# Kernel optimization log

Hardware: AMD Instinct MI355X
Metric: run time of the kernel (lower is better)

The kernel has to match this reference:

```python
import jax, jax.numpy as jnp
import numpy as np

N, E, H, G, L = 50000, 640000, 128, 8, 3

def setup_inputs() -> dict:
    key = jax.random.key(0)
    ks = jax.random.split(key, 10)
    s = 1.0 / np.sqrt(H)
    return {
        "x": jax.random.normal(ks[0], (N, H), jnp.float32),
        "query": jax.random.normal(ks[1], (G, H), jnp.float32),
        "Wl": jax.random.normal(ks[2], (L, H, H), jnp.float32) * s,
        "bl": jax.random.normal(ks[3], (L, H), jnp.float32) * s,
        "Wr": jax.random.normal(ks[4], (L, H, H), jnp.float32) * s,
        "Wlin": jax.random.normal(ks[5], (H, H), jnp.float32) * s,
        "blin": jax.random.normal(ks[6], (H,), jnp.float32) * s,
        "edge_index": jax.random.randint(ks[7], (2, E), 0, N, jnp.int64),
        "batch_vec": jnp.sort(jax.random.randint(ks[8], (N,), 0, G, jnp.int64)),
    }

def reference(x, query, Wl, bl, Wr, Wlin, blin, edge_index, batch_vec):
    src, dst = edge_index[0], edge_index[1]
    n = x.shape[0]
    for i in range(L):
        # SAGEConv(aggr='max'): gather neighbor feats, scatter-max to dst
        m = jax.ops.segment_max(x[src], dst, num_segments=n)  # [N,H]
        m = jnp.where(jnp.isfinite(m), m, 0.0)  # isolated nodes -> 0 (PyG)
        x = jax.nn.relu(m @ Wl[i].T + bl[i] + x @ Wr[i].T)
    x = x @ Wlin.T + blin  # encoder final linear
    # cosine scoring per graph, vectorized via batch_vec
    xn = x / jnp.linalg.norm(x, axis=1, keepdims=True).clip(1e-12)
    qn = query / jnp.linalg.norm(query, axis=1, keepdims=True).clip(1e-12)
    scores = jnp.sum(xn * qn[batch_vec], axis=1)  # [N]
    return scores
```

## Files before the change

### kernel.cpp

```cpp
#include <hip/hip_runtime.h>
#include <math.h>

#define H 128

typedef _Float16 half8 __attribute__((ext_vector_type(8)));
typedef float f32x16 __attribute__((ext_vector_type(16)));
typedef int int4v __attribute__((ext_vector_type(4)));

__device__ __forceinline__ half8 h8max(half8 a, half8 b) {
#if defined(__has_builtin) && __has_builtin(__builtin_elementwise_max)
    return __builtin_elementwise_max(a, b);
#else
    half8 r;
#pragma unroll
    for (int j = 0; j < 8; ++j) r[j] = a[j] > b[j] ? a[j] : b[j];
    return r;
#endif
}

__device__ __forceinline__ half8 h8shfl_xor(half8 v, int mask) {
    int4v iv;
    __builtin_memcpy(&iv, &v, 16);
#pragma unroll
    for (int j = 0; j < 4; ++j) iv[j] = __shfl_xor(iv[j], mask, 64);
    half8 r;
    __builtin_memcpy(&r, &iv, 16);
    return r;
}


__global__ __launch_bounds__(256) void scan_atomic(const int* __restrict__ deg,
                                                   int* __restrict__ offsets,
                                                   int* __restrict__ gcur, int N) {
    __shared__ int buf[256];
    __shared__ int sbase;
    int tid = threadIdx.x;
    int i = blockIdx.x * 256 + tid;
    int v = (i < N) ? deg[i] : 0;
    int incl = v;
    buf[tid] = v;
    __syncthreads();
#pragma unroll
    for (int off = 1; off < 256; off <<= 1) {
        int t = (tid >= off) ? buf[tid - off] : 0;
        __syncthreads();
        incl += t;
        buf[tid] = incl;
        __syncthreads();
    }
    if (tid == 255) sbase = atomicAdd(gcur, incl);
    __syncthreads();
    if (i < N) offsets[i] = sbase + incl - v;
}

__global__ __launch_bounds__(256) void fill_adj(const int* __restrict__ ei, int E,
                                                const int* __restrict__ offsets,
                                                int* __restrict__ cursor,
                                                int* __restrict__ adj) {
    int e = blockIdx.x * 256 + threadIdx.x;
    if (e < E) {
        int s = ei[e];
        int d = ei[E + e];
        int pos = atomicAdd(&cursor[d], 1);
        adj[offsets[d] + pos] = s;
    }
}


__global__ __launch_bounds__(256) void prep_all(
    const int* __restrict__ ei, int E, int* __restrict__ deg,
    const float* __restrict__ x, const float* __restrict__ query,
    const float* __restrict__ Wl, const float* __restrict__ Wr,
    const float* __restrict__ Wlin, _Float16* __restrict__ xh,
    _Float16* __restrict__ wimg, float* __restrict__ qn, int n8, int HB, int SB,
    int WB) {
    int b = blockIdx.x;
    int tid = threadIdx.x;
    if (b < HB) {
        int e = b * 256 + tid;
        if (e < E) atomicAdd(&deg[ei[E + e]], 1);
    } else if (b < HB + SB) {
        int i = (b - HB) * 256 + tid;
        if (i < n8) {
            const float4* x4 = (const float4*)x;
            float4 u = x4[(size_t)i * 2], v = x4[(size_t)i * 2 + 1];
            float f[8] = {u.x, u.y, u.z, u.w, v.x, v.y, v.z, v.w};
            half8 h;
#pragma unroll
            for (int j = 0; j < 8; ++j) h[j] = (_Float16)f[j];
            *(half8*)(xh + (size_t)i * 8) = h;
        }
    } else if (b < HB + SB + WB) {
        int gidx = (b - HB - SB) * 256 + tid;
        if (gidx < 7 * 2048) {
            int mat = gidx / 2048;
            int rem = gidx - mat * 2048;
            int n = rem >> 4;
            int g = rem & 15;
            const float* src = (mat == 6) ? Wlin
                             : ((mat & 1) ? Wr + (mat >> 1) * H * H
                                          : Wl + (mat >> 1) * H * H);
            const float* p = src + n * H + g * 8;
            half8 h, l;
#pragma unroll
            for (int j = 0; j < 8; ++j) {
                float v = p[j];
                _Float16 hh = (_Float16)v;
                h[j] = hh;
                l[j] = (_Float16)(v - (float)hh);
            }
            int kc4 = g >> 2, gpc = g & 3;
            int posB = (gpc + (n & 3) + ((n >> 2) & 3)) & 3;
            size_t base = (size_t)mat * 32768 + (size_t)kc4 * 8192 + n * 32 + posB * 8;
            *(half8*)(wimg + base) = h;
            *(half8*)(wimg + base + 4096) = l;
        }
    } else {
        int g = b - HB - SB - WB;
        __shared__ float part[4];
        float v = (tid < 128) ? query[g * H + tid] : 0.f;
        float ss = v * v;
#pragma unroll
        for (int off = 32; off > 0; off >>= 1) ss += __shfl_xor(ss, off, 64);
        if ((tid & 63) == 0) part[tid >> 6] = ss;
        __syncthreads();
        float tot = part[0] + part[1];
        if (tid < 128) qn[g * H + tid] = v / fmaxf(sqrtf(tot), 1e-12f);
    }
}


__global__ __launch_bounds__(256) void layer_fused3(
    const half8* __restrict__ Xh, const int* __restrict__ deg,
    const int* __restrict__ offsets, const int* __restrict__ adj,
    const _Float16* __restrict__ Bimg, const float* __restrict__ bias,
    _Float16* __restrict__ Yh, int N) {
    __shared__ __align__(16) _Float16 sU[8192];
    __shared__ __align__(16) _Float16 sB[8192];

    int tid = threadIdx.x;
    int w = tid >> 6;
    int lane = tid & 63;
    int l31 = lane & 31;
    int lhi = lane >> 5;
    int ws = w >> 1;
    int wc = w & 1;
    int n0 = blockIdx.x * 64;

    {
        int sub = lane >> 4;
        int lf = lane & 15;
        const _Float16 ni = (_Float16)(-INFINITY);
        const half8 ninf = {ni, ni, ni, ni, ni, ni, ni, ni};
        const half8 hz = {(_Float16)0.f, (_Float16)0.f, (_Float16)0.f, (_Float16)0.f,
                          (_Float16)0.f, (_Float16)0.f, (_Float16)0.f, (_Float16)0.f};
        int nd = n0 + w * 16 + lf;
        int ndc = nd < N ? nd : N - 1;
        int e0v = offsets[ndc];
        int degv = (nd < N) ? deg[ndc] : 0;

        for (int i = 0; i < 16; ++i) {
            int e0 = __shfl(e0v, i, 64);
            int d = __shfl(degv, i, 64);
            int row = w * 16 + i;
            half8 acc = ninf;
            for (int base = 0; base < d; base += 16) {
                half8 v[4];
#pragma unroll
                for (int q = 0; q < 4; ++q) {
                    int j = base + q * 4 + sub;
                    int idx = adj[e0 + (j < d ? j : d - 1)];
                    v[q] = Xh[(size_t)idx * 16 + lf];
                }
                acc = h8max(acc, h8max(h8max(v[0], v[1]), h8max(v[2], v[3])));
            }
            acc = h8max(acc, h8shfl_xor(acc, 16));
            acc = h8max(acc, h8shfl_xor(acc, 32));
            if (d == 0) acc = hz;
            if (sub == 0) *(half8*)&sU[row * 128 + (lf ^ (row & 15)) * 8] = acc;
        }
    }
    __syncthreads();

    f32x16 acc[2];
#pragma unroll
    for (int nt = 0; nt < 2; ++nt) {
        float bv = bias[wc * 64 + nt * 32 + l31];
#pragma unroll
        for (int r = 0; r < 16; ++r) acc[nt][r] = bv;
    }

    int rl = ws * 32 + l31;

    for (int kc4 = 0; kc4 < 4; ++kc4) {
        if (kc4) __syncthreads();
        {
            const half8* bsrc = (const half8*)(Bimg + (size_t)kc4 * 8192);
            half8* bdst = (half8*)sB;
#pragma unroll
            for (int i = 0; i < 4; ++i) bdst[tid + i * 256] = bsrc[tid + i * 256];
        }
        __syncthreads();
#pragma unroll
        for (int ks = 0; ks < 2; ++ks) {
            int g16 = kc4 * 4 + ks * 2 + lhi;
            int posA = g16 ^ (rl & 15);
            half8 ah = *(const half8*)&sU[rl * 128 + posA * 8];
#pragma unroll
            for (int nt = 0; nt < 2; ++nt) {
                int n = wc * 64 + nt * 32 + l31;
                int gpc = ks * 2 + lhi;
                int posB = (gpc + (n & 3) + ((n >> 2) & 3)) & 3;
                half8 bh = *(const half8*)&sB[n * 32 + posB * 8];
                half8 bl = *(const half8*)&sB[4096 + n * 32 + posB * 8];
                acc[nt] = __builtin_amdgcn_mfma_f32_32x32x16_f16(ah, bh, acc[nt], 0, 0, 0);
                acc[nt] = __builtin_amdgcn_mfma_f32_32x32x16_f16(ah, bl, acc[nt], 0, 0, 0);
            }
        }
    }

    for (int kc4 = 0; kc4 < 4; ++kc4) {
        __syncthreads();
        {
            const half8* bsrc = (const half8*)(Bimg + 32768 + (size_t)kc4 * 8192);
            half8* bdst = (half8*)sB;
#pragma unroll
            for (int i = 0; i < 4; ++i) bdst[tid + i * 256] = bsrc[tid + i * 256];
        }
        if ((kc4 & 1) == 0) {
            int kc64 = kc4 >> 1;
#pragma unroll
            for (int i = 0; i < 2; ++i) {
                int idx = tid + i * 256;
                int row = idx >> 3;
                int gp8 = idx & 7;
                int n = n0 + row;
                half8 h = {(_Float16)0.f, (_Float16)0.f, (_Float16)0.f, (_Float16)0.f,
                           (_Float16)0.f, (_Float16)0.f, (_Float16)0.f, (_Float16)0.f};
                if (n < N) h = Xh[(size_t)n * 16 + kc64 * 8 + gp8];
                int pos8 = (gp8 + (row & 7) + ((row >> 3) & 7)) & 7;
                *(half8*)&sU[row * 72 + pos8 * 8] = h;
            }
        }
        __syncthreads();
#pragma unroll
        for (int ks = 0; ks < 2; ++ks) {
            int gp8 = (kc4 & 1) * 4 + ks * 2 + lhi;
            int posA8 = (gp8 + (rl & 7) + ((rl >> 3) & 7)) & 7;
            half8 ah = *(const half8*)&sU[rl * 72 + posA8 * 8];
#pragma unroll
            for (int nt = 0; nt < 2; ++nt) {
                int n = wc * 64 + nt * 32 + l31;
                int gpc = ks * 2 + lhi;
                int posB = (gpc + (n & 3) + ((n >> 2) & 3)) & 3;
                half8 bh = *(const half8*)&sB[n * 32 + posB * 8];
                half8 bl = *(const half8*)&sB[4096 + n * 32 + posB * 8];
                acc[nt] = __builtin_amdgcn_mfma_f32_32x32x16_f16(ah, bh, acc[nt], 0, 0, 0);
                acc[nt] = __builtin_amdgcn_mfma_f32_32x32x16_f16(ah, bl, acc[nt], 0, 0, 0);
            }
        }
    }

#pragma unroll
    for (int r = 0; r < 16; ++r) {
        int row = n0 + ws * 32 + (r & 3) + 8 * (r >> 2) + 4 * lhi;
        if (row < N) {
#pragma unroll
            for (int nt = 0; nt < 2; ++nt) {
                int col = wc * 64 + nt * 32 + l31;
                Yh[(size_t)row * H + col] = (_Float16)fmaxf(acc[nt][r], 0.f);
            }
        }
    }
}


__global__ __launch_bounds__(256) void final_mfma6(
    const half8* __restrict__ Xh, const _Float16* __restrict__ Bimg,
    const float* __restrict__ blin, const float* __restrict__ qn,
    const int* __restrict__ bv, float* __restrict__ out, int N) {
    __shared__ __align__(16) _Float16 sA[9216];
    __shared__ __align__(16) _Float16 sB[8192];

    int tid = threadIdx.x;
    int w = tid >> 6;
    int lane = tid & 63;
    int l31 = lane & 31;
    int lhi = lane >> 5;
    int n0 = blockIdx.x * 128;

    int arow = n0 + w * 32 + l31;
    arow = arow < N ? arow : N - 1;
    int gl = bv[arow];

    f32x16 acc[4];
#pragma unroll
    for (int nt = 0; nt < 4; ++nt) {
        float b = blin[nt * 32 + l31];
#pragma unroll
        for (int r = 0; r < 16; ++r) acc[nt][r] = b;
    }

    int rl = w * 32 + l31;

    for (int kc4 = 0; kc4 < 4; ++kc4) {
        if (kc4) __syncthreads();
        {
            const half8* bsrc = (const half8*)(Bimg + (size_t)kc4 * 8192);
            half8* bdst = (half8*)sB;
#pragma unroll
            for (int i = 0; i < 4; ++i) bdst[tid + i * 256] = bsrc[tid + i * 256];
        }
        if ((kc4 & 1) == 0) {
            int kc64 = kc4 >> 1;
#pragma unroll
            for (int i = 0; i < 4; ++i) {
                int idx = tid + i * 256;
                int row = idx >> 3;
                int gp8 = idx & 7;
                int n = n0 + row;
                half8 h = {(_Float16)0.f, (_Float16)0.f, (_Float16)0.f, (_Float16)0.f,
                           (_Float16)0.f, (_Float16)0.f, (_Float16)0.f, (_Float16)0.f};
                if (n < N) h = Xh[(size_t)n * 16 + kc64 * 8 + gp8];
                int pos8 = (gp8 + (row & 7) + ((row >> 3) & 7)) & 7;
                *(half8*)&sA[row * 72 + pos8 * 8] = h;
            }
        }
        __syncthreads();
#pragma unroll
        for (int ks = 0; ks < 2; ++ks) {
            int gp8 = (kc4 & 1) * 4 + ks * 2 + lhi;
            int posA8 = (gp8 + (rl & 7) + ((rl >> 3) & 7)) & 7;
            half8 ah = *(const half8*)&sA[rl * 72 + posA8 * 8];
#pragma unroll
            for (int nt = 0; nt < 4; ++nt) {
                int n = nt * 32 + l31;
                int gpc = ks * 2 + lhi;
                int posB = (gpc + (n & 3) + ((n >> 2) & 3)) & 3;
                half8 bh = *(const half8*)&sB[n * 32 + posB * 8];
                half8 bl = *(const half8*)&sB[4096 + n * 32 + posB * 8];
                acc[nt] = __builtin_amdgcn_mfma_f32_32x32x16_f16(ah, bh, acc[nt], 0, 0, 0);
                acc[nt] = __builtin_amdgcn_mfma_f32_32x32x16_f16(ah, bl, acc[nt], 0, 0, 0);
            }
        }
    }

#pragma unroll
    for (int r = 0; r < 16; ++r) {
        int rloc = (r & 3) + 8 * (r >> 2) + 4 * lhi;
        int row = n0 + w * 32 + rloc;
        int g = __shfl(gl, rloc, 32);
        float ss = 0.f, sd = 0.f;
#pragma unroll
        for (int nt = 0; nt < 4; ++nt) {
            float y = acc[nt][r];
            float q = qn[(size_t)g * H + nt * 32 + l31];
            ss = fmaf(y, y, ss);
            sd = fmaf(y, q, sd);
        }
#pragma unroll
        for (int off = 1; off <= 16; off <<= 1) {
            ss += __shfl_xor(ss, off, 64);
            sd += __shfl_xor(sd, off, 64);
        }
        if (l31 == 0 && row < N) out[row] = sd / fmaxf(sqrtf(ss), 1e-12f);
    }
}


extern "C" void kernel_launch(void* const* d_in, const int* in_sizes, int n_in,
                              void* d_out, int out_size, void* d_ws, size_t ws_size,
                              hipStream_t stream) {
    const float* x = (const float*)d_in[0];
    const float* query = (const float*)d_in[1];
    const float* Wl = (const float*)d_in[2];
    const float* bl = (const float*)d_in[3];
    const float* Wr = (const float*)d_in[4];
    const float* Wlin = (const float*)d_in[5];
    const float* blin = (const float*)d_in[6];
    const int* ei = (const int*)d_in[7];
    const int* bv = (const int*)d_in[8];
    float* out = (float*)d_out;

    const int N = in_sizes[0] / H;
    const int E = in_sizes[7] / 2;
    const int G = in_sizes[1] / H;

    char* p = (char*)d_ws;
    auto alloc = [&](size_t bytes) {
        char* r = p;
        p += (bytes + 255) & ~(size_t)255;
        return r;
    };
    int* deg = (int*)alloc((size_t)(2 * N + 1) * sizeof(int));
    int* cursor = deg + N;
    int* gcur = deg + 2 * N;
    int* offsets = (int*)alloc((size_t)N * sizeof(int));
    int* adj = (int*)alloc((size_t)E * sizeof(int));
    float* qn = (float*)alloc((size_t)G * H * sizeof(float));
    _Float16* wimg = (_Float16*)alloc((size_t)7 * 32768 * sizeof(_Float16));
    size_t actH = (size_t)N * H * sizeof(_Float16);
    _Float16* xah = (_Float16*)alloc(actH);
    _Float16* xbh = (_Float16*)alloc(actH);

    hipMemsetAsync(deg, 0, (size_t)(2 * N + 1) * sizeof(int), stream);

    const int n8 = N * H / 8;
    const int HB = (E + 255) / 256;
    const int SB = (n8 + 255) / 256;
    const int WB = (7 * 2048 + 255) / 256;
    prep_all<<<HB + SB + WB + G, 256, 0, stream>>>(ei, E, deg, x, query, Wl, Wr,
                                                   Wlin, xah, wimg, qn, n8, HB,
                                                   SB, WB);
    scan_atomic<<<(N + 255) / 256, 256, 0, stream>>>(deg, offsets, gcur, N);
    fill_adj<<<(E + 255) / 256, 256, 0, stream>>>(ei, E, offsets, cursor, adj);

    const int NGm = (N + 63) / 64;
    const int NGf = (N + 127) / 128;

    layer_fused3<<<NGm, 256, 0, stream>>>(
        (const half8*)xah, deg, offsets, adj, wimg + (size_t)0 * 65536,
        bl + 0 * H, xbh, N);
    layer_fused3<<<NGm, 256, 0, stream>>>(
        (const half8*)xbh, deg, offsets, adj, wimg + (size_t)1 * 65536,
        bl + 1 * H, xah, N);
    layer_fused3<<<NGm, 256, 0, stream>>>(
        (const half8*)xah, deg, offsets, adj, wimg + (size_t)2 * 65536,
        bl + 2 * H, xbh, N);
    final_mfma6<<<NGf, 256, 0, stream>>>(
        (const half8*)xbh, wimg + (size_t)6 * 32768, blin, qn, bv, out, N);
}
```

Baseline: 282.7 us.

## Fuse final linear and cosine scoring into last layer; register-cached adjacency gather

The last SAGE layer kernel is templated so that its FINAL variant writes the ReLU output to shared memory and immediately runs the final linear GEMM and cosine scoring. This removes the separate final kernel and the round trip of the activation through global memory. Separately, when all 16 nodes in a wave group have degree at most 32, adjacency indices are loaded once into registers and distributed via shuffles. That path issues a fixed 8 gathers per node, which adds memory-level parallelism at the cost of some redundant clamped loads.

Result: no change. 283.8 us (+0.4%).

```diff
diff --git a/kernel.cpp b/kernel.cpp
--- a/kernel.cpp
+++ b/kernel.cpp
@@ -130,11 +130,14 @@
 }
 
 
-__global__ __launch_bounds__(256) void layer_fused3(
+template <bool FINAL>
+__global__ __launch_bounds__(256) void layer_fused(
     const half8* __restrict__ Xh, const int* __restrict__ deg,
     const int* __restrict__ offsets, const int* __restrict__ adj,
     const _Float16* __restrict__ Bimg, const float* __restrict__ bias,
-    _Float16* __restrict__ Yh, int N) {
+    _Float16* __restrict__ Yh, const _Float16* __restrict__ BimgF,
+    const float* __restrict__ blin, const float* __restrict__ qn,
+    const int* __restrict__ bv, float* __restrict__ out, int N) {
     __shared__ __align__(16) _Float16 sU[8192];
     __shared__ __align__(16) _Float16 sB[8192];
 
@@ -159,25 +162,65 @@
         int e0v = offsets[ndc];
         int degv = (nd < N) ? deg[ndc] : 0;
 
-        for (int i = 0; i < 16; ++i) {
-            int e0 = __shfl(e0v, i, 64);
-            int d = __shfl(degv, i, 64);
-            int row = w * 16 + i;
-            half8 acc = ninf;
-            for (int base = 0; base < d; base += 16) {
-                half8 v[4];
-#pragma unroll
-                for (int q = 0; q < 4; ++q) {
-                    int j = base + q * 4 + sub;
-                    int idx = adj[e0 + (j < d ? j : d - 1)];
+        int dmx = degv;
+#pragma unroll
+        for (int off = 1; off <= 8; off <<= 1) {
+            int t = __shfl_xor(dmx, off, 64);
+            dmx = t > dmx ? t : dmx;
+        }
+
+        if (dmx <= 32) {
+            int adjf[8];
+#pragma unroll
+            for (int rr = 0; rr < 8; ++rr) {
+                int i = 2 * rr + (lane >> 5);
+                int e0 = __shfl(e0v, i, 64);
+                int d = __shfl(degv, i, 64);
+                int s = lane & 31;
+                int p = d > 0 ? e0 + (s < d ? s : d - 1) : 0;
+                adjf[rr] = adj[p];
+            }
+#pragma unroll
+            for (int i = 0; i < 16; ++i) {
+                int d = __shfl(degv, i, 64);
+                int dm1 = d > 0 ? d - 1 : 0;
+                half8 v[8];
+#pragma unroll
+                for (int q = 0; q < 8; ++q) {
+                    int j = q * 4 + sub;
+                    int jc = j < d ? j : dm1;
+                    int idx = __shfl(adjf[i >> 1], ((i & 1) << 5) | jc, 64);
                     v[q] = Xh[(size_t)idx * 16 + lf];
                 }
-                acc = h8max(acc, h8max(h8max(v[0], v[1]), h8max(v[2], v[3])));
-            }
-            acc = h8max(acc, h8shfl_xor(acc, 16));
-            acc = h8max(acc, h8shfl_xor(acc, 32));
-            if (d == 0) acc = hz;
-            if (sub == 0) *(half8*)&sU[row * 128 + (lf ^ (row & 15)) * 8] = acc;
+                half8 acc = h8max(h8max(h8max(v[0], v[1]), h8max(v[2], v[3])),
+                                  h8max(h8max(v[4], v[5]), h8max(v[6], v[7])));
+                acc = h8max(acc, h8shfl_xor(acc, 16));
+                acc = h8max(acc, h8shfl_xor(acc, 32));
+                if (d == 0) acc = hz;
+                int row = w * 16 + i;
+                if (sub == 0) *(half8*)&sU[row * 128 + ((lf ^ (row & 15)) << 3)] = acc;
+            }
+        } else {
+            for (int i = 0; i < 16; ++i) {
+                int e0 = __shfl(e0v, i, 64);
+                int d = __shfl(degv, i, 64);
+                int row = w * 16 + i;
+                half8 acc = ninf;
+                for (int base = 0; base < d; base += 16) {
+                    half8 v[4];
+#pragma unroll
+                    for (int q = 0; q < 4; ++q) {
+                        int j = base + q * 4 + sub;
+                        int idx = adj[e0 + (j < d ? j : d - 1)];
+                        v[q] = Xh[(size_t)idx * 16 + lf];
+                    }
+                    acc = h8max(acc, h8max(h8max(v[0], v[1]), h8max(v[2], v[3])));
+                }
+                acc = h8max(acc, h8shfl_xor(acc, 16));
+                acc = h8max(acc, h8shfl_xor(acc, 32));
+                if (d == 0) acc = hz;
+                if (sub == 0) *(half8*)&sU[row * 128 + ((lf ^ (row & 15)) << 3)] = acc;
+            }
         }
     }
     __syncthreads();
@@ -185,9 +228,9 @@
     f32x16 acc[2];
 #pragma unroll
     for (int nt = 0; nt < 2; ++nt) {
-        float bv = bias[wc * 64 + nt * 32 + l31];
-#pragma unroll
-        for (int r = 0; r < 16; ++r) acc[nt][r] = bv;
+        float bvv = bias[wc * 64 + nt * 32 + l31];
+#pragma unroll
+        for (int r = 0; r < 16; ++r) acc[nt][r] = bvv;
     }
 
     int rl = ws * 32 + l31;
@@ -212,9 +255,9 @@
                 int gpc = ks * 2 + lhi;
                 int posB = (gpc + (n & 3) + ((n >> 2) & 3)) & 3;
                 half8 bh = *(const half8*)&sB[n * 32 + posB * 8];
-                half8 bl = *(const half8*)&sB[4096 + n * 32 + posB * 8];
+                half8 bl2 = *(const half8*)&sB[4096 + n * 32 + posB * 8];
                 acc[nt] = __builtin_amdgcn_mfma_f32_32x32x16_f16(ah, bh, acc[nt], 0, 0, 0);
-                acc[nt] = __builtin_amdgcn_mfma_f32_32x32x16_f16(ah, bl, acc[nt], 0, 0, 0);
+                acc[nt] = __builtin_amdgcn_mfma_f32_32x32x16_f16(ah, bl2, acc[nt], 0, 0, 0);
             }
         }
     }
@@ -254,116 +297,110 @@
                 int gpc = ks * 2 + lhi;
                 int posB = (gpc + (n & 3) + ((n >> 2) & 3)) & 3;
                 half8 bh = *(const half8*)&sB[n * 32 + posB * 8];
-                half8 bl = *(const half8*)&sB[4096 + n * 32 + posB * 8];
+                half8 bl2 = *(const half8*)&sB[4096 + n * 32 + posB * 8];
                 acc[nt] = __builtin_amdgcn_mfma_f32_32x32x16_f16(ah, bh, acc[nt], 0, 0, 0);
-                acc[nt] = __builtin_amdgcn_mfma_f32_32x32x16_f16(ah, bl, acc[nt], 0, 0, 0);
-            }
-        }
-    }
-
-#pragma unroll
-    for (int r = 0; r < 16; ++r) {
-        int row = n0 + ws * 32 + (r & 3) + 8 * (r >> 2) + 4 * lhi;
-        if (row < N) {
+                acc[nt] = __builtin_amdgcn_mfma_f32_32x32x16_f16(ah, bl2, acc[nt], 0, 0, 0);
+            }
+        }
+    }
+
+    if constexpr (!FINAL) {
+#pragma unroll
+        for (int r = 0; r < 16; ++r) {
+            int row = n0 + ws * 32 + (r & 3) + 8 * (r >> 2) + 4 * lhi;
+            if (row < N) {
+#pragma unroll
+                for (int nt = 0; nt < 2; ++nt) {
+                    int col = wc * 64 + nt * 32 + l31;
+                    Yh[(size_t)row * H + col] = (_Float16)fmaxf(acc[nt][r], 0.f);
+                }
+            }
+        }
+    } else {
+        __syncthreads();
+#pragma unroll
+        for (int r = 0; r < 16; ++r) {
+            int rloc = ws * 32 + (r & 3) + 8 * (r >> 2) + 4 * lhi;
 #pragma unroll
             for (int nt = 0; nt < 2; ++nt) {
-                int col = wc * 64 + nt * 32 + l31;
-                Yh[(size_t)row * H + col] = (_Float16)fmaxf(acc[nt][r], 0.f);
-            }
-        }
-    }
-}
-
-
-__global__ __launch_bounds__(256) void final_mfma6(
-    const half8* __restrict__ Xh, const _Float16* __restrict__ Bimg,
-    const float* __restrict__ blin, const float* __restrict__ qn,
-    const int* __restrict__ bv, float* __restrict__ out, int N) {
-    __shared__ __align__(16) _Float16 sA[9216];
-    __shared__ __align__(16) _Float16 sB[8192];
-
-    int tid = threadIdx.x;
-    int w = tid >> 6;
-    int lane = tid & 63;
-    int l31 = lane & 31;
-    int lhi = lane >> 5;
-    int n0 = blockIdx.x * 128;
-
-    int arow = n0 + w * 32 + l31;
-    arow = arow < N ? arow : N - 1;
-    int gl = bv[arow];
-
-    f32x16 acc[4];
-#pragma unroll
-    for (int nt = 0; nt < 4; ++nt) {
-        float b = blin[nt * 32 + l31];
-#pragma unroll
-        for (int r = 0; r < 16; ++r) acc[nt][r] = b;
-    }
-
-    int rl = w * 32 + l31;
-
-    for (int kc4 = 0; kc4 < 4; ++kc4) {
-        if (kc4) __syncthreads();
-        {
-            const half8* bsrc = (const half8*)(Bimg + (size_t)kc4 * 8192);
-            half8* bdst = (half8*)sB;
-#pragma unroll
-            for (int i = 0; i < 4; ++i) bdst[tid + i * 256] = bsrc[tid + i * 256];
-        }
-        if ((kc4 & 1) == 0) {
-            int kc64 = kc4 >> 1;
-#pragma unroll
-            for (int i = 0; i < 4; ++i) {
-                int idx = tid + i * 256;
-                int row = idx >> 3;
-                int gp8 = idx & 7;
-                int n = n0 + row;
-                half8 h = {(_Float16)0.f, (_Float16)0.f, (_Float16)0.f, (_Float16)0.f,
-                           (_Float16)0.f, (_Float16)0.f, (_Float16)0.f, (_Float16)0.f};
-                if (n < N) h = Xh[(size_t)n * 16 + kc64 * 8 + gp8];
-                int pos8 = (gp8 + (row & 7) + ((row >> 3) & 7)) & 7;
-                *(half8*)&sA[row * 72 + pos8 * 8] = h;
-            }
-        }
-        __syncthreads();
-#pragma unroll
-        for (int ks = 0; ks < 2; ++ks) {
-            int gp8 = (kc4 & 1) * 4 + ks * 2 + lhi;
-            int posA8 = (gp8 + (rl & 7) + ((rl >> 3) & 7)) & 7;
-            half8 ah = *(const half8*)&sA[rl * 72 + posA8 * 8];
-#pragma unroll
-            for (int nt = 0; nt < 4; ++nt) {
-                int n = nt * 32 + l31;
-                int gpc = ks * 2 + lhi;
-                int posB = (gpc + (n & 3) + ((n >> 2) & 3)) & 3;
-                half8 bh = *(const half8*)&sB[n * 32 + posB * 8];
-                half8 bl = *(const half8*)&sB[4096 + n * 32 + posB * 8];
-                acc[nt] = __builtin_amdgcn_mfma_f32_32x32x16_f16(ah, bh, acc[nt], 0, 0, 0);
-                acc[nt] = __builtin_amdgcn_mfma_f32_32x32x16_f16(ah, bl, acc[nt], 0, 0, 0);
-            }
-        }
-    }
-
-#pragma unroll
-    for (int r = 0; r < 16; ++r) {
-        int rloc = (r & 3) + 8 * (r >> 2) + 4 * lhi;
-        int row = n0 + w * 32 + rloc;
-        int g = __shfl(gl, rloc, 32);
-        float ss = 0.f, sd = 0.f;
-#pragma unroll
-        for (int nt = 0; nt < 4; ++nt) {
-            float y = acc[nt][r];
-            float q = qn[(size_t)g * H + nt * 32 + l31];
-            ss = fmaf(y, y, ss);
-            sd = fmaf(y, q, sd);
-        }
-#pragma unroll
-        for (int off = 1; off <= 16; off <<= 1) {
-            ss += __shfl_xor(ss, off, 64);
-            sd += __shfl_xor(sd, off, 64);
-        }
-        if (l31 == 0 && row < N) out[row] = sd / fmaxf(sqrtf(ss), 1e-12f);
+                int c = wc * 64 + nt * 32 + l31;
+                sU[rloc * 128 + (((c >> 3) ^ (rloc & 15)) << 3) + (c & 7)] =
+                    (_Float16)fmaxf(acc[nt][r], 0.f);
+            }
+        }
+
+        f32x16 acc2[2];
+#pragma unroll
+        for (int nt = 0; nt < 2; ++nt) {
+            float b = blin[wc * 64 + nt * 32 + l31];
+#pragma unroll
+            for (int r = 0; r < 16; ++r) acc2[nt][r] = b;
+        }
+
+        for (int kc4 = 0; kc4 < 4; ++kc4) {
+            __syncthreads();
+            {
+                const half8* bsrc = (const half8*)(BimgF + (size_t)kc4 * 8192);
+                half8* bdst = (half8*)sB;
+#pragma unroll
+                for (int i = 0; i < 4; ++i) bdst[tid + i * 256] = bsrc[tid + i * 256];
+            }
+            __syncthreads();
+#pragma unroll
+            for (int ks = 0; ks < 2; ++ks) {
+                int g16 = kc4 * 4 + ks * 2 + lhi;
+                int posA = g16 ^ (rl & 15);
+                half8 ah = *(const half8*)&sU[rl * 128 + posA * 8];
+#pragma unroll
+                for (int nt = 0; nt < 2; ++nt) {
+                    int n = wc * 64 + nt * 32 + l31;
+                    int gpc = ks * 2 + lhi;
+                    int posB = (gpc + (n & 3) + ((n >> 2) & 3)) & 3;
+                    half8 bh = *(const half8*)&sB[n * 32 + posB * 8];
+                    half8 bl2 = *(const half8*)&sB[4096 + n * 32 + posB * 8];
+                    acc2[nt] = __builtin_amdgcn_mfma_f32_32x32x16_f16(ah, bh, acc2[nt], 0, 0, 0);
+                    acc2[nt] = __builtin_amdgcn_mfma_f32_32x32x16_f16(ah, bl2, acc2[nt], 0, 0, 0);
+                }
+            }
+        }
+
+        int rgl = n0 + ws * 32 + l31;
+        rgl = rgl < N ? rgl : N - 1;
+        int gl = bv[rgl];
+        __syncthreads();
+        float* sP = (float*)sB;
+#pragma unroll
+        for (int r = 0; r < 16; ++r) {
+            int rloc = (r & 3) + 8 * (r >> 2) + 4 * lhi;
+            int g = __shfl(gl, rloc, 32);
+            float ss = 0.f, sd = 0.f;
+#pragma unroll
+            for (int nt = 0; nt < 2; ++nt) {
+                float y = acc2[nt][r];
+                float q = qn[(size_t)g * H + wc * 64 + nt * 32 + l31];
+                ss = fmaf(y, y, ss);
+                sd = fmaf(y, q, sd);
+            }
+#pragma unroll
+            for (int off = 1; off <= 16; off <<= 1) {
+                ss += __shfl_xor(ss, off, 64);
+                sd += __shfl_xor(sd, off, 64);
+            }
+            if (l31 == 0) {
+                int rowl = ws * 32 + rloc;
+                sP[rowl * 4 + wc * 2] = ss;
+                sP[rowl * 4 + wc * 2 + 1] = sd;
+            }
+        }
+        __syncthreads();
+        if (tid < 64) {
+            int row = n0 + tid;
+            if (row < N) {
+                float ss = sP[tid * 4] + sP[tid * 4 + 2];
+                float sd = sP[tid * 4 + 1] + sP[tid * 4 + 3];
+                out[row] = sd / fmaxf(sqrtf(ss), 1e-12f);
+            }
+        }
     }
 }
 
@@ -416,17 +453,14 @@
     fill_adj<<<(E + 255) / 256, 256, 0, stream>>>(ei, E, offsets, cursor, adj);
 
     const int NGm = (N + 63) / 64;
-    const int NGf = (N + 127) / 128;
-
-    layer_fused3<<<NGm, 256, 0, stream>>>(
+
+    layer_fused<false><<<NGm, 256, 0, stream>>>(
         (const half8*)xah, deg, offsets, adj, wimg + (size_t)0 * 65536,
-        bl + 0 * H, xbh, N);
-    layer_fused3<<<NGm, 256, 0, stream>>>(
+        bl + 0 * H, xbh, nullptr, nullptr, nullptr, nullptr, nullptr, N);
+    layer_fused<false><<<NGm, 256, 0, stream>>>(
         (const half8*)xbh, deg, offsets, adj, wimg + (size_t)1 * 65536,
-        bl + 1 * H, xah, N);
-    layer_fused3<<<NGm, 256, 0, stream>>>(
+        bl + 1 * H, xah, nullptr, nullptr, nullptr, nullptr, nullptr, N);
+    layer_fused<true><<<NGm, 256, 0, stream>>>(
         (const half8*)xah, deg, offsets, adj, wimg + (size_t)2 * 65536,
-        bl + 2 * H, xbh, N);
-    final_mfma6<<<NGf, 256, 0, stream>>>(
-        (const half8*)xbh, wimg + (size_t)6 * 32768, blin, qn, bv, out, N);
-}
+        bl + 2 * H, nullptr, wimg + (size_t)6 * 32768, blin, qn, bv, out, N);
+}
```

## Shrink layer tile to 32 nodes, read weights from global, batch adjacency loads

Applied to the files above, without the earlier changes.

The fused SAGE layer kernel now handles 32 nodes per block instead of 64 and drops the shared-memory weight staging. Each wave owns one 32-column output tile and reads its B fragments straight from global memory (through cache), which halves LDS use and removes most barriers so more blocks fit per CU (launch bounds 8). For groups whose maximum degree is at most 32, the gather preloads adjacency indices into registers and distributes them with shuffles, issuing 8 neighbour loads at once. The cost is redundant global/L2 weight reads in every block and a divergent fallback path for high-degree nodes.

Result: faster. 272.7 us (-3.5%).

```diff
diff --git a/kernel.cpp b/kernel.cpp
--- a/kernel.cpp
+++ b/kernel.cpp
@@ -130,22 +130,19 @@
 }
 
 
-__global__ __launch_bounds__(256) void layer_fused3(
+__global__ __launch_bounds__(256, 8) void layer_fused(
     const half8* __restrict__ Xh, const int* __restrict__ deg,
     const int* __restrict__ offsets, const int* __restrict__ adj,
     const _Float16* __restrict__ Bimg, const float* __restrict__ bias,
     _Float16* __restrict__ Yh, int N) {
-    __shared__ __align__(16) _Float16 sU[8192];
-    __shared__ __align__(16) _Float16 sB[8192];
+    __shared__ __align__(16) _Float16 sU[4096];
 
     int tid = threadIdx.x;
     int w = tid >> 6;
     int lane = tid & 63;
     int l31 = lane & 31;
     int lhi = lane >> 5;
-    int ws = w >> 1;
-    int wc = w & 1;
-    int n0 = blockIdx.x * 64;
+    int n0 = blockIdx.x * 32;
 
     {
         int sub = lane >> 4;
@@ -154,123 +151,137 @@
         const half8 ninf = {ni, ni, ni, ni, ni, ni, ni, ni};
         const half8 hz = {(_Float16)0.f, (_Float16)0.f, (_Float16)0.f, (_Float16)0.f,
                           (_Float16)0.f, (_Float16)0.f, (_Float16)0.f, (_Float16)0.f};
-        int nd = n0 + w * 16 + lf;
+        int nd = n0 + w * 8 + (lf & 7);
         int ndc = nd < N ? nd : N - 1;
         int e0v = offsets[ndc];
         int degv = (nd < N) ? deg[ndc] : 0;
 
-        for (int i = 0; i < 16; ++i) {
-            int e0 = __shfl(e0v, i, 64);
-            int d = __shfl(degv, i, 64);
-            int row = w * 16 + i;
-            half8 acc = ninf;
-            for (int base = 0; base < d; base += 16) {
-                half8 v[4];
-#pragma unroll
-                for (int q = 0; q < 4; ++q) {
-                    int j = base + q * 4 + sub;
-                    int idx = adj[e0 + (j < d ? j : d - 1)];
+        int dmx = degv;
+#pragma unroll
+        for (int off = 1; off <= 8; off <<= 1) {
+            int t = __shfl_xor(dmx, off, 64);
+            dmx = t > dmx ? t : dmx;
+        }
+
+        if (dmx <= 32) {
+            int adjf[4];
+#pragma unroll
+            for (int rr = 0; rr < 4; ++rr) {
+                int i = 2 * rr + (lane >> 5);
+                int e0 = __shfl(e0v, i, 64);
+                int d = __shfl(degv, i, 64);
+                int s = lane & 31;
+                int p = d > 0 ? e0 + (s < d ? s : d - 1) : 0;
+                adjf[rr] = adj[p];
+            }
+#pragma unroll
+            for (int i = 0; i < 8; ++i) {
+                int d = __shfl(degv, i, 64);
+                int dm1 = d > 0 ? d - 1 : 0;
+                half8 v[8];
+#pragma unroll
+                for (int q = 0; q < 8; ++q) {
+                    int j = q * 4 + sub;
+                    int jc = j < d ? j : dm1;
+                    int idx = __shfl(adjf[i >> 1], ((i & 1) << 5) | jc, 64);
                     v[q] = Xh[(size_t)idx * 16 + lf];
                 }
-                acc = h8max(acc, h8max(h8max(v[0], v[1]), h8max(v[2], v[3])));
-            }
-            acc = h8max(acc, h8shfl_xor(acc, 16));
-            acc = h8max(acc, h8shfl_xor(acc, 32));
-            if (d == 0) acc = hz;
-            if (sub == 0) *(half8*)&sU[row * 128 + (lf ^ (row & 15)) * 8] = acc;
+                half8 acc = h8max(h8max(h8max(v[0], v[1]), h8max(v[2], v[3])),
+                                  h8max(h8max(v[4], v[5]), h8max(v[6], v[7])));
+                acc = h8max(acc, h8shfl_xor(acc, 16));
+                acc = h8max(acc, h8shfl_xor(acc, 32));
+                if (d == 0) acc = hz;
+                int row = w * 8 + i;
+                if (sub == 0) *(half8*)&sU[row * 128 + ((lf ^ (row & 15)) << 3)] = acc;
+            }
+        } else {
+            for (int i = 0; i < 8; ++i) {
+                int e0 = __shfl(e0v, i, 64);
+                int d = __shfl(degv, i, 64);
+                int row = w * 8 + i;
+                half8 acc = ninf;
+                for (int base = 0; base < d; base += 16) {
+                    half8 v[4];
+#pragma unroll
+                    for (int q = 0; q < 4; ++q) {
+                        int j = base + q * 4 + sub;
+                        int idx = adj[e0 + (j < d ? j : d - 1)];
+                        v[q] = Xh[(size_t)idx * 16 + lf];
+                    }
+                    acc = h8max(acc, h8max(h8max(v[0], v[1]), h8max(v[2], v[3])));
+                }
+                acc = h8max(acc, h8shfl_xor(acc, 16));
+                acc = h8max(acc, h8shfl_xor(acc, 32));
+                if (d == 0) acc = hz;
+                if (sub == 0) *(half8*)&sU[row * 128 + ((lf ^ (row & 15)) << 3)] = acc;
+            }
         }
     }
     __syncthreads();
 
-    f32x16 acc[2];
-#pragma unroll
-    for (int nt = 0; nt < 2; ++nt) {
-        float bv = bias[wc * 64 + nt * 32 + l31];
-#pragma unroll
-        for (int r = 0; r < 16; ++r) acc[nt][r] = bv;
-    }
-
-    int rl = ws * 32 + l31;
-
+    f32x16 acc;
+    {
+        float bvv = bias[w * 32 + l31];
+#pragma unroll
+        for (int r = 0; r < 16; ++r) acc[r] = bvv;
+    }
+
+    int rl = l31;
+    int n = w * 32 + l31;
+
+#pragma unroll
     for (int kc4 = 0; kc4 < 4; ++kc4) {
-        if (kc4) __syncthreads();
-        {
-            const half8* bsrc = (const half8*)(Bimg + (size_t)kc4 * 8192);
-            half8* bdst = (half8*)sB;
-#pragma unroll
-            for (int i = 0; i < 4; ++i) bdst[tid + i * 256] = bsrc[tid + i * 256];
-        }
-        __syncthreads();
+        const _Float16* Bc = Bimg + (size_t)kc4 * 8192;
 #pragma unroll
         for (int ks = 0; ks < 2; ++ks) {
             int g16 = kc4 * 4 + ks * 2 + lhi;
             int posA = g16 ^ (rl & 15);
             half8 ah = *(const half8*)&sU[rl * 128 + posA * 8];
-#pragma unroll
-            for (int nt = 0; nt < 2; ++nt) {
-                int n = wc * 64 + nt * 32 + l31;
+            int gpc = ks * 2 + lhi;
+            int posB = (gpc + (n & 3) + ((n >> 2) & 3)) & 3;
+            half8 bh = *(const half8*)&Bc[n * 32 + posB * 8];
+            half8 bl2 = *(const half8*)&Bc[4096 + n * 32 + posB * 8];
+            acc = __builtin_amdgcn_mfma_f32_32x32x16_f16(ah, bh, acc, 0, 0, 0);
+            acc = __builtin_amdgcn_mfma_f32_32x32x16_f16(ah, bl2, acc, 0, 0, 0);
+        }
+    }
+
+#pragma unroll
+    for (int kc64 = 0; kc64 < 2; ++kc64) {
+        __syncthreads();
+        {
+            int row = tid >> 3;
+            int gp8 = tid & 7;
+            int nn = n0 + row;
+            half8 h = {(_Float16)0.f, (_Float16)0.f, (_Float16)0.f, (_Float16)0.f,
+                       (_Float16)0.f, (_Float16)0.f, (_Float16)0.f, (_Float16)0.f};
+            if (nn < N) h = Xh[(size_t)nn * 16 + kc64 * 8 + gp8];
+            int pos8 = (gp8 + (row & 7) + ((row >> 3) & 7)) & 7;
+            *(half8*)&sU[row * 72 + pos8 * 8] = h;
+        }
+        __syncthreads();
+#pragma unroll
+        for (int kc4 = 2 * kc64; kc4 < 2 * kc64 + 2; ++kc4) {
+            const _Float16* Bc = Bimg + 32768 + (size_t)kc4 * 8192;
+#pragma unroll
+            for (int ks = 0; ks < 2; ++ks) {
+                int gp8 = (kc4 & 1) * 4 + ks * 2 + lhi;
+                int posA8 = (gp8 + (rl & 7) + ((rl >> 3) & 7)) & 7;
+                half8 ah = *(const half8*)&sU[rl * 72 + posA8 * 8];
                 int gpc = ks * 2 + lhi;
                 int posB = (gpc + (n & 3) + ((n >> 2) & 3)) & 3;
-                half8 bh = *(const half8*)&sB[n * 32 + posB * 8];
-                half8 bl = *(const half8*)&sB[4096 + n * 32 + posB * 8];
-                acc[nt] = __builtin_amdgcn_mfma_f32_32x32x16_f16(ah, bh, acc[nt], 0, 0, 0);
-                acc[nt] = __builtin_amdgcn_mfma_f32_32x32x16_f16(ah, bl, acc[nt], 0, 0, 0);
-            }
-        }
-    }
-
-    for (int kc4 = 0; kc4 < 4; ++kc4) {
-        __syncthreads();
-        {
-            const half8* bsrc = (const half8*)(Bimg + 32768 + (size_t)kc4 * 8192);
-            half8* bdst = (half8*)sB;
-#pragma unroll
-            for (int i = 0; i < 4; ++i) bdst[tid + i * 256] = bsrc[tid + i * 256];
-        }
-        if ((kc4 & 1) == 0) {
-            int kc64 = kc4 >> 1;
-#pragma unroll
-            for (int i = 0; i < 2; ++i) {
-                int idx = tid + i * 256;
-                int row = idx >> 3;
-                int gp8 = idx & 7;
-                int n = n0 + row;
-                half8 h = {(_Float16)0.f, (_Float16)0.f, (_Float16)0.f, (_Float16)0.f,
-                           (_Float16)0.f, (_Float16)0.f, (_Float16)0.f, (_Float16)0.f};
-                if (n < N) h = Xh[(size_t)n * 16 + kc64 * 8 + gp8];
-                int pos8 = (gp8 + (row & 7) + ((row >> 3) & 7)) & 7;
-                *(half8*)&sU[row * 72 + pos8 * 8] = h;
-            }
-        }
-        __syncthreads();
-#pragma unroll
-        for (int ks = 0; ks < 2; ++ks) {
-            int gp8 = (kc4 & 1) * 4 + ks * 2 + lhi;
-            int posA8 = (gp8 + (rl & 7) + ((rl >> 3) & 7)) & 7;
-            half8 ah = *(const half8*)&sU[rl * 72 + posA8 * 8];
-#pragma unroll
-            for (int nt = 0; nt < 2; ++nt) {
-                int n = wc * 64 + nt * 32 + l31;
-                int gpc = ks * 2 + lhi;
-                int posB = (gpc + (n & 3) + ((n >> 2) & 3)) & 3;
-                half8 bh = *(const half8*)&sB[n * 32 + posB * 8];
-                half8 bl = *(const half8*)&sB[4096 + n * 32 + posB * 8];
-                acc[nt] = __builtin_amdgcn_mfma_f32_32x32x16_f16(ah, bh, acc[nt], 0, 0, 0);
-                acc[nt] = __builtin_amdgcn_mfma_f32_32x32x16_f16(ah, bl, acc[nt], 0, 0, 0);
+                half8 bh = *(const half8*)&Bc[n * 32 + posB * 8];
+                half8 bl2 = *(const half8*)&Bc[4096 + n * 32 + posB * 8];
+                acc = __builtin_amdgcn_mfma_f32_32x32x16_f16(ah, bh, acc, 0, 0, 0);
+                acc = __builtin_amdgcn_mfma_f32_32x32x16_f16(ah, bl2, acc, 0, 0, 0);
             }
         }
     }
 
 #pragma unroll
     for (int r = 0; r < 16; ++r) {
-        int row = n0 + ws * 32 + (r & 3) + 8 * (r >> 2) + 4 * lhi;
-        if (row < N) {
-#pragma unroll
-            for (int nt = 0; nt < 2; ++nt) {
-                int col = wc * 64 + nt * 32 + l31;
-                Yh[(size_t)row * H + col] = (_Float16)fmaxf(acc[nt][r], 0.f);
-            }
-        }
+        int row = n0 + (r & 3) + 8 * (r >> 2) + 4 * lhi;
+        if (row < N) Yh[(size_t)row * H + n] = (_Float16)fmaxf(acc[r], 0.f);
     }
 }
 
@@ -318,10 +329,10 @@
                 int idx = tid + i * 256;
                 int row = idx >> 3;
                 int gp8 = idx & 7;
-                int n = n0 + row;
+                int nn = n0 + row;
                 half8 h = {(_Float16)0.f, (_Float16)0.f, (_Float16)0.f, (_Float16)0.f,
                            (_Float16)0.f, (_Float16)0.f, (_Float16)0.f, (_Float16)0.f};
-                if (n < N) h = Xh[(size_t)n * 16 + kc64 * 8 + gp8];
+                if (nn < N) h = Xh[(size_t)nn * 16 + kc64 * 8 + gp8];
                 int pos8 = (gp8 + (row & 7) + ((row >> 3) & 7)) & 7;
                 *(half8*)&sA[row * 72 + pos8 * 8] = h;
             }
@@ -334,13 +345,13 @@
             half8 ah = *(const half8*)&sA[rl * 72 + posA8 * 8];
 #pragma unroll
             for (int nt = 0; nt < 4; ++nt) {
-                int n = nt * 32 + l31;
+                int nn = nt * 32 + l31;
                 int gpc = ks * 2 + lhi;
-                int posB = (gpc + (n & 3) + ((n >> 2) & 3)) & 3;
-                half8 bh = *(const half8*)&sB[n * 32 + posB * 8];
-                half8 bl = *(const half8*)&sB[4096 + n * 32 + posB * 8];
+                int posB = (gpc + (nn & 3) + ((nn >> 2) & 3)) & 3;
+                half8 bh = *(const half8*)&sB[nn * 32 + posB * 8];
+                half8 bl2 = *(const half8*)&sB[4096 + nn * 32 + posB * 8];
                 acc[nt] = __builtin_amdgcn_mfma_f32_32x32x16_f16(ah, bh, acc[nt], 0, 0, 0);
-                acc[nt] = __builtin_amdgcn_mfma_f32_32x32x16_f16(ah, bl, acc[nt], 0, 0, 0);
+                acc[nt] = __builtin_amdgcn_mfma_f32_32x32x16_f16(ah, bl2, acc[nt], 0, 0, 0);
             }
         }
     }
@@ -415,16 +426,16 @@
     scan_atomic<<<(N + 255) / 256, 256, 0, stream>>>(deg, offsets, gcur, N);
     fill_adj<<<(E + 255) / 256, 256, 0, stream>>>(ei, E, offsets, cursor, adj);
 
-    const int NGm = (N + 63) / 64;
+    const int NGm = (N + 31) / 32;
     const int NGf = (N + 127) / 128;
 
-    layer_fused3<<<NGm, 256, 0, stream>>>(
+    layer_fused<<<NGm, 256, 0, stream>>>(
         (const half8*)xah, deg, offsets, adj, wimg + (size_t)0 * 65536,
         bl + 0 * H, xbh, N);
-    layer_fused3<<<NGm, 256, 0, stream>>>(
+    layer_fused<<<NGm, 256, 0, stream>>>(
         (const half8*)xbh, deg, offsets, adj, wimg + (size_t)1 * 65536,
         bl + 1 * H, xah, N);
-    layer_fused3<<<NGm, 256, 0, stream>>>(
+    layer_fused<<<NGm, 256, 0, stream>>>(
         (const half8*)xah, deg, offsets, adj, wimg + (size_t)2 * 65536,
         bl + 2 * H, xbh, N);
     final_mfma6<<<NGf, 256, 0, stream>>>(
```
